# Performance work log

Measured on AMD Instinct MI355X. Metric: run time of the kernel, lower is better.

Reference implementation:

```python
import jax, jax.numpy as jnp
import numpy as np

EMBED_DIM = 1024
NUM_HEADS = 16
HEAD_DIM = EMBED_DIM // NUM_HEADS
SCALING = HEAD_DIM ** -0.5
TGT, BSZ = 1024, 4


def setup_inputs() -> dict:
    key = jax.random.key(0)
    ks = jax.random.split(key, 8)
    query = jax.random.normal(ks[0], (TGT, BSZ, EMBED_DIM), dtype=jnp.float32)
    key_padding_mask = jax.random.randint(ks[1], (BSZ, TGT), 0, 2, dtype=jnp.int32)
    attn_mask = jax.random.normal(ks[2], (TGT, TGT), dtype=jnp.float32)
    attn_bias = jax.random.normal(ks[3], (BSZ * NUM_HEADS, TGT, TGT), dtype=jnp.float32)
    W_in = jax.random.normal(ks[4], (3 * EMBED_DIM, EMBED_DIM), dtype=jnp.float32) * 0.02
    b_in = jnp.zeros((3 * EMBED_DIM,), dtype=jnp.float32)
    W_out = jax.random.normal(ks[5], (EMBED_DIM, EMBED_DIM), dtype=jnp.float32) * 0.02
    b_out = jnp.zeros((EMBED_DIM,), dtype=jnp.float32)
    return {"query": query, "key_padding_mask": key_padding_mask,
            "attn_mask": attn_mask, "attn_bias": attn_bias,
            "W_in": W_in, "b_in": b_in, "W_out": W_out, "b_out": b_out}


def reference(query, key_padding_mask, attn_mask, attn_bias, W_in, b_in, W_out, b_out):
    tgt_len, bsz, embed_dim = query.shape
    # in_proj: (T,B,C) @ W_in.T -> (T,B,3C), chunk into q,k,v
    qkv = jnp.einsum('tbc,ec->tbe', query, W_in) + b_in
    q, k, v = jnp.split(qkv, 3, axis=-1)
    # reshape to (B*H, T, D)
    def to_bh(x):
        return x.reshape(tgt_len, bsz * NUM_HEADS, HEAD_DIM).transpose(1, 0, 2)
    q = to_bh(q) * SCALING
    k = to_bh(k)
    v = to_bh(v)
    src_len = k.shape[1]
    # scores: (B*H, T, S)
    attn_weights = jnp.einsum('ntd,nsd->nts', q, k)
    attn_weights = attn_weights + attn_mask[None, :, :]
    kpm = key_padding_mask.astype(bool)  # (B, S), True = pad
    aw = attn_weights.reshape(bsz, NUM_HEADS, tgt_len, src_len)
    aw = jnp.where(kpm[:, None, None, :], -jnp.inf, aw)
    attn_weights = aw.reshape(bsz * NUM_HEADS, tgt_len, src_len)
    attn_weights = attn_weights + attn_bias
    attn_probs = jax.nn.softmax(attn_weights, axis=-1)
    attn = jnp.einsum('nts,nsd->ntd', attn_probs, v)
    attn = attn.transpose(1, 0, 2).reshape(tgt_len, bsz, embed_dim)
    out = jnp.einsum('tbc,ec->tbe', attn, W_out) + b_out
    return out
```

## Files before the change

### kernel.cpp

```cpp
#include <hip/hip_runtime.h>

#define T_LEN 1024
#define B_SZ 4
#define EMB 1024
#define NH 16
#define HD 64
#define QKV_LD 3072

typedef _Float16 f16;
typedef __attribute__((ext_vector_type(8))) _Float16 f16x8;
typedef __attribute__((ext_vector_type(4))) _Float16 f16x4;
typedef __attribute__((ext_vector_type(4))) float f32x4;

__device__ __forceinline__ void gload16(const f16* g, f16* l) {
    __builtin_amdgcn_global_load_lds(
        (const __attribute__((address_space(1))) void*)g,
        (__attribute__((address_space(3))) void*)l, 16, 0, 0);
}

#define N4_Q  (4096 * 1024 / 4)
#define N4_WI (3072 * 1024 / 4)
#define N4_WO (1024 * 1024 / 4)
__global__ __launch_bounds__(256) void cvt_all(
    const float* __restrict__ q, const float* __restrict__ wi,
    const float* __restrict__ wo, f16* __restrict__ q16,
    f16* __restrict__ wi16, f16* __restrict__ wo16)
{
    int i = blockIdx.x * 256 + threadIdx.x;
    const float* src; f16* dst; int off;
    if (i < N4_Q)             { src = q;  dst = q16;  off = i; }
    else if (i < N4_Q + N4_WI){ src = wi; dst = wi16; off = i - N4_Q; }
    else                      { src = wo; dst = wo16; off = i - N4_Q - N4_WI; }
    float4 v = ((const float4*)src)[off];
    f16x4 h = { (f16)v.x, (f16)v.y, (f16)v.z, (f16)v.w };
    ((f16x4*)dst)[off] = h;
}

template<bool OUT_HALF>
__global__ __launch_bounds__(256) void gemm_ct(
    const f16* __restrict__ Wt, const f16* __restrict__ Xa,
    const float* __restrict__ bias, void* __restrict__ Out,
    int K, int ldo)
{
    __shared__ f16 As[128 * 32];
    __shared__ f16 Bs[128 * 32];
    const int tid = threadIdx.x;
    const int wv = tid >> 6, lane = tid & 63;
    const int lq = lane & 15, quad = lane >> 4;
    const int m0 = blockIdx.x * 128, n0 = blockIdx.y * 128;
    const int wm = (wv >> 1) * 64, wn = (wv & 1) * 64;

    const int s1 = tid, s2 = 256 + tid;
    const f16* a1 = Wt + (size_t)(m0 + (s1 >> 2)) * K + (s1 & 3) * 8;
    const f16* a2 = Wt + (size_t)(m0 + (s2 >> 2)) * K + (s2 & 3) * 8;
    const f16* b1 = Xa + (size_t)(n0 + (s1 >> 2)) * K + (s1 & 3) * 8;
    const f16* b2 = Xa + (size_t)(n0 + (s2 >> 2)) * K + (s2 & 3) * 8;
    f16* lA1 = As + s1 * 8; f16* lA2 = As + s2 * 8;
    f16* lB1 = Bs + s1 * 8; f16* lB2 = Bs + s2 * 8;

    f32x4 acc[4][4];
#pragma unroll
    for (int i = 0; i < 4; ++i)
#pragma unroll
        for (int j = 0; j < 4; ++j) acc[i][j] = (f32x4){0.f, 0.f, 0.f, 0.f};

    for (int k0 = 0; k0 < K; k0 += 32) {
        __syncthreads();
        gload16(a1 + k0, lA1);
        gload16(a2 + k0, lA2);
        gload16(b1 + k0, lB1);
        gload16(b2 + k0, lB2);
        __syncthreads();
        f16x8 af[4], bf[4];
#pragma unroll
        for (int t = 0; t < 4; ++t) {
            af[t] = *(const f16x8*)&As[(wm + t * 16 + lq) * 32 + quad * 8];
            bf[t] = *(const f16x8*)&Bs[(wn + t * 16 + lq) * 32 + quad * 8];
        }
#pragma unroll
        for (int mt = 0; mt < 4; ++mt)
#pragma unroll
            for (int nt = 0; nt < 4; ++nt)
                acc[mt][nt] = __builtin_amdgcn_mfma_f32_16x16x32_f16(
                    af[mt], bf[nt], acc[mt][nt], 0, 0, 0);
    }

#pragma unroll
    for (int mt = 0; mt < 4; ++mt) {
        const int e0 = m0 + wm + mt * 16 + quad * 4;
        const float4 bb = *(const float4*)(bias + e0);
#pragma unroll
        for (int nt = 0; nt < 4; ++nt) {
            const int xr = n0 + wn + nt * 16 + lq;
            if (OUT_HALF) {
                f16x4 h = { (f16)(acc[mt][nt][0] + bb.x), (f16)(acc[mt][nt][1] + bb.y),
                            (f16)(acc[mt][nt][2] + bb.z), (f16)(acc[mt][nt][3] + bb.w) };
                *(f16x4*)((f16*)Out + (size_t)xr * ldo + e0) = h;
            } else {
                float4 o = { acc[mt][nt][0] + bb.x, acc[mt][nt][1] + bb.y,
                             acc[mt][nt][2] + bb.z, acc[mt][nt][3] + bb.w };
                *(float4*)((float*)Out + (size_t)xr * ldo + e0) = o;
            }
        }
    }
}

__global__ __launch_bounds__(256) void vtrans(
    const f16* __restrict__ qkv, f16* __restrict__ Vth)
{
    __shared__ f16 Ls[256 * 66];
    const int bh = blockIdx.x;
    const int t0 = blockIdx.y * 256;
    const int b = bh >> 4, hh = bh & 15;
    const int tid = threadIdx.x;

#pragma unroll
    for (int p = 0; p < 8; ++p) {
        const int g = p * 2048 + tid * 8;
        const int ti = g >> 6, dj = g & 63;
        f16x8 v = *(const f16x8*)(qkv + (size_t)((t0 + ti) * 4 + b) * QKV_LD + 2048 + hh * 64 + dj);
        *(f16x8*)&Ls[ti * 66 + dj] = v;
    }
    __syncthreads();
#pragma unroll
    for (int p = 0; p < 8; ++p) {
        const int g = p * 2048 + tid * 8;
        const int d = g >> 8, tt = g & 255;
        f16x8 o;
#pragma unroll
        for (int j = 0; j < 8; ++j) o[j] = Ls[(tt + j) * 66 + d];
        *(f16x8*)(Vth + (size_t)bh * 65536 + (size_t)d * 1024 + t0 + tt) = o;
    }
}

__global__ __launch_bounds__(256, 3) void attn_v5(
    const f16* __restrict__ qkv, const f16* __restrict__ Vth,
    const int* __restrict__ kpm, const float* __restrict__ attn_mask,
    const float* __restrict__ attn_bias, f16* __restrict__ ctx)
{
    const int LDP = 72;
    __shared__ f16 Ps[4 * 16 * LDP];

    const int tid = threadIdx.x;
    const int wv = tid >> 6, lane = tid & 63;
    const int lq = lane & 15, quad = lane >> 4;
    const int q0 = blockIdx.x * 64;
    const int bh = blockIdx.y;
    const int b = bh >> 4, hh = bh & 15;
    f16* Pw = Ps + wv * 16 * LDP;

    const int t = q0 + wv * 16 + lq;
    const float* mrow = attn_mask + (size_t)t * T_LEN;
    const float* brow = attn_bias + ((size_t)bh * T_LEN + t) * T_LEN;
    const int* kpr = kpm + b * T_LEN;
    const f16* Vb = Vth + (size_t)bh * 65536;

    f16x8 bq[2];
    {
        const f16* qrow = qkv + (size_t)(t * 4 + b) * QKV_LD + hh * 64;
        bq[0] = *(const f16x8*)(qrow + quad * 8);
        bq[1] = *(const f16x8*)(qrow + 32 + quad * 8);
    }

    float m_i = -1e30f, l_i = 0.0f;
    f32x4 O[4];
#pragma unroll
    for (int dt = 0; dt < 4; ++dt) O[dt] = (f32x4){0.f, 0.f, 0.f, 0.f};

    f32x4 bcur[4];
#pragma unroll
    for (int st = 0; st < 4; ++st)
        bcur[st] = __builtin_nontemporal_load((const f32x4*)(brow + st * 16 + quad * 4));

#pragma unroll 1
    for (int sh = 0; sh < T_LEN; sh += 64) {
        f32x4 bnxt[4];
        if (sh + 64 < T_LEN) {
#pragma unroll
            for (int st = 0; st < 4; ++st)
                bnxt[st] = __builtin_nontemporal_load(
                    (const f32x4*)(brow + sh + 64 + st * 16 + quad * 4));
        }

        f16x8 ak[2][4];
#pragma unroll
        for (int ks = 0; ks < 2; ++ks)
#pragma unroll
            for (int st = 0; st < 4; ++st)
                ak[ks][st] = *(const f16x8*)(qkv
                    + (size_t)((sh + st * 16 + lq) * 4 + b) * QKV_LD
                    + EMB + hh * 64 + ks * 32 + quad * 8);

        f32x4 m4[4]; int4 kp4[4];
#pragma unroll
        for (int st = 0; st < 4; ++st) {
            const int sb = sh + st * 16 + quad * 4;
            m4[st] = *(const f32x4*)(mrow + sb);
            kp4[st] = *(const int4*)(kpr + sb);
        }

        f32x4 sacc[4];
#pragma unroll
        for (int st = 0; st < 4; ++st) sacc[st] = (f32x4){0.f, 0.f, 0.f, 0.f};
        __builtin_amdgcn_s_setprio(1);
#pragma unroll
        for (int ks = 0; ks < 2; ++ks)
#pragma unroll
            for (int st = 0; st < 4; ++st)
                sacc[st] = __builtin_amdgcn_mfma_f32_16x16x32_f16(
                    ak[ks][st], bq[ks], sacc[st], 0, 0, 0);
        __builtin_amdgcn_s_setprio(0);

        f16x8 av[2][4];
#pragma unroll
        for (int ks = 0; ks < 2; ++ks)
#pragma unroll
            for (int dt = 0; dt < 4; ++dt)
                av[ks][dt] = *(const f16x8*)(Vb + (size_t)(dt * 16 + lq) * 1024
                                             + sh + ks * 32 + quad * 8);

        float sv[4][4];
        float rm = -1e30f;
#pragma unroll
        for (int st = 0; st < 4; ++st) {
            const int kv[4] = {kp4[st].x, kp4[st].y, kp4[st].z, kp4[st].w};
#pragma unroll
            for (int r = 0; r < 4; ++r) {
                const float x = sacc[st][r] * 0.125f + m4[st][r] + bcur[st][r];
                sv[st][r] = kv[r] ? -1e30f : x;
                rm = fmaxf(rm, sv[st][r]);
            }
        }
        rm = fmaxf(rm, __shfl_xor(rm, 16));
        rm = fmaxf(rm, __shfl_xor(rm, 32));

        const bool skip = __all(rm <= m_i + 8.0f);
        float alpha;
        if (skip) {
            alpha = 1.0f;
        } else {
            const float mn = fmaxf(m_i, rm);
            alpha = __expf(m_i - mn);
            m_i = mn;
        }

        __builtin_amdgcn_wave_barrier();
        float rs = 0.0f;
#pragma unroll
        for (int st = 0; st < 4; ++st) {
            f16x4 pv;
#pragma unroll
            for (int r = 0; r < 4; ++r) {
                const float p = __expf(sv[st][r] - m_i);
                rs += p;
                pv[r] = (f16)p;
            }
            *(f16x4*)&Pw[lq * LDP + st * 16 + quad * 4] = pv;
        }
        rs += __shfl_xor(rs, 16);
        rs += __shfl_xor(rs, 32);
        l_i = l_i * alpha + rs;

        if (!skip) {
            float aB[4];
#pragma unroll
            for (int r = 0; r < 4; ++r) aB[r] = __shfl(alpha, quad * 4 + r, 16);
#pragma unroll
            for (int dt = 0; dt < 4; ++dt)
#pragma unroll
                for (int r = 0; r < 4; ++r) O[dt][r] *= aB[r];
        }

        __builtin_amdgcn_wave_barrier();

        __builtin_amdgcn_s_setprio(1);
#pragma unroll
        for (int ks = 0; ks < 2; ++ks) {
            const f16x8 ap = *(const f16x8*)&Pw[lq * LDP + ks * 32 + quad * 8];
#pragma unroll
            for (int dt = 0; dt < 4; ++dt)
                O[dt] = __builtin_amdgcn_mfma_f32_16x16x32_f16(
                    ap, av[ks][dt], O[dt], 0, 0, 0);
        }
        __builtin_amdgcn_s_setprio(0);

#pragma unroll
        for (int st = 0; st < 4; ++st) bcur[st] = bnxt[st];
    }

    float lB[4];
#pragma unroll
    for (int r = 0; r < 4; ++r) lB[r] = __shfl(l_i, quad * 4 + r, 16);
#pragma unroll
    for (int r = 0; r < 4; ++r) {
        const float inv = 1.0f / lB[r];
        const int tt = q0 + wv * 16 + quad * 4 + r;
#pragma unroll
        for (int dt = 0; dt < 4; ++dt)
            ctx[((size_t)tt * B_SZ + b) * EMB + hh * HD + dt * 16 + lq] = (f16)(O[dt][r] * inv);
    }
}

extern "C" void kernel_launch(void* const* d_in, const int* in_sizes, int n_in,
                              void* d_out, int out_size, void* d_ws, size_t ws_size,
                              hipStream_t stream)
{
    const float* query     = (const float*)d_in[0];
    const int*   kpm       = (const int*)  d_in[1];
    const float* attn_mask = (const float*)d_in[2];
    const float* attn_bias = (const float*)d_in[3];
    const float* W_in      = (const float*)d_in[4];
    const float* b_in      = (const float*)d_in[5];
    const float* W_out     = (const float*)d_in[6];
    const float* b_out     = (const float*)d_in[7];
    float* out = (float*)d_out;

    f16* q16    = (f16*)d_ws;
    f16* win16  = q16    + (size_t)4096 * 1024;
    f16* wout16 = win16  + (size_t)3072 * 1024;
    f16* qkv16  = wout16 + (size_t)1024 * 1024;
    f16* Vth    = qkv16  + (size_t)4096 * 3072;
    f16* ctx16  = Vth    + (size_t)64 * 65536;

    cvt_all<<<(N4_Q + N4_WI + N4_WO) / 256, 256, 0, stream>>>(
        query, W_in, W_out, q16, win16, wout16);

    dim3 g1(3072 / 128, 4096 / 128);
    gemm_ct<true><<<g1, 256, 0, stream>>>(win16, q16, b_in, qkv16, 1024, QKV_LD);

    dim3 gv(64, 4);
    vtrans<<<gv, 256, 0, stream>>>(qkv16, Vth);

    dim3 g2(T_LEN / 64, B_SZ * NH);
    attn_v5<<<g2, 256, 0, stream>>>(qkv16, Vth, kpm, attn_mask, attn_bias, ctx16);

    dim3 g3(1024 / 128, 4096 / 128);
    gemm_ct<false><<<g3, 256, 0, stream>>>(wout16, ctx16, b_out, out, 1024, 1024);
}
```

Measured before the change: 579.2 us.

## Split attention key range across two wave groups and prefold padding into mask

The attention kernel now uses 512 threads per block. Two groups of four waves each process half of the key sequence, and their partial softmax states (max, sum, output) are merged through shared memory at the end. A new prepass kernel folds the key padding mask into a per-batch copy of the additive attention mask. This removes the int mask loads and selects from the inner loop. The split is meant to raise parallelism and hide the latency of the memory-bound bias stream, at the cost of an extra 16MB mask buffer, an extra kernel launch and the merge step.

```diff
diff --git a/kernel.cpp b/kernel.cpp
--- a/kernel.cpp
+++ b/kernel.cpp
@@ -34,6 +34,21 @@
     float4 v = ((const float4*)src)[off];
     f16x4 h = { (f16)v.x, (f16)v.y, (f16)v.z, (f16)v.w };
     ((f16x4*)dst)[off] = h;
+}
+
+__global__ __launch_bounds__(256) void maskfold(
+    const float* __restrict__ attn_mask, const int* __restrict__ kpm,
+    float* __restrict__ maskc)
+{
+    const int i = blockIdx.x * 256 + threadIdx.x;
+    const int s4 = i & 255;
+    const int t = (i >> 8) & 1023;
+    const int b = i >> 18;
+    float4 m = ((const float4*)(attn_mask + (size_t)t * T_LEN))[s4];
+    int4 k = ((const int4*)(kpm + b * T_LEN))[s4];
+    float4 o = { k.x ? -1e30f : m.x, k.y ? -1e30f : m.y,
+                 k.z ? -1e30f : m.z, k.w ? -1e30f : m.w };
+    ((float4*)(maskc + ((size_t)b * T_LEN + t) * T_LEN))[s4] = o;
 }
 
 template<bool OUT_HALF>
@@ -133,26 +148,30 @@
     }
 }
 
-__global__ __launch_bounds__(256, 3) void attn_v5(
+__global__ __launch_bounds__(512, 6) void attn_v6(
     const f16* __restrict__ qkv, const f16* __restrict__ Vth,
-    const int* __restrict__ kpm, const float* __restrict__ attn_mask,
-    const float* __restrict__ attn_bias, f16* __restrict__ ctx)
+    const float* __restrict__ maskc, const float* __restrict__ attn_bias,
+    f16* __restrict__ ctx)
 {
     const int LDP = 72;
-    __shared__ f16 Ps[4 * 16 * LDP];
+    __shared__ f16 Ps[8 * 16 * LDP];
+    __shared__ float Osh[4][16][66];
+    __shared__ float Msh[4][16];
+    __shared__ float Lsh[4][16];
 
     const int tid = threadIdx.x;
     const int wv = tid >> 6, lane = tid & 63;
+    const int wq = wv & 3, half = wv >> 2;
     const int lq = lane & 15, quad = lane >> 4;
     const int q0 = blockIdx.x * 64;
     const int bh = blockIdx.y;
     const int b = bh >> 4, hh = bh & 15;
     f16* Pw = Ps + wv * 16 * LDP;
 
-    const int t = q0 + wv * 16 + lq;
-    const float* mrow = attn_mask + (size_t)t * T_LEN;
+    const int t = q0 + wq * 16 + lq;
+    const int S0 = half * 512;
+    const float* mrow = maskc + ((size_t)b * T_LEN + t) * T_LEN;
     const float* brow = attn_bias + ((size_t)bh * T_LEN + t) * T_LEN;
-    const int* kpr = kpm + b * T_LEN;
     const f16* Vb = Vth + (size_t)bh * 65536;
 
     f16x8 bq[2];
@@ -170,12 +189,13 @@
     f32x4 bcur[4];
 #pragma unroll
     for (int st = 0; st < 4; ++st)
-        bcur[st] = __builtin_nontemporal_load((const f32x4*)(brow + st * 16 + quad * 4));
+        bcur[st] = __builtin_nontemporal_load(
+            (const f32x4*)(brow + S0 + st * 16 + quad * 4));
 
 #pragma unroll 1
-    for (int sh = 0; sh < T_LEN; sh += 64) {
+    for (int sh = S0; sh < S0 + 512; sh += 64) {
         f32x4 bnxt[4];
-        if (sh + 64 < T_LEN) {
+        if (sh + 64 < S0 + 512) {
 #pragma unroll
             for (int st = 0; st < 4; ++st)
                 bnxt[st] = __builtin_nontemporal_load(
@@ -191,13 +211,10 @@
                     + (size_t)((sh + st * 16 + lq) * 4 + b) * QKV_LD
                     + EMB + hh * 64 + ks * 32 + quad * 8);
 
-        f32x4 m4[4]; int4 kp4[4];
-#pragma unroll
-        for (int st = 0; st < 4; ++st) {
-            const int sb = sh + st * 16 + quad * 4;
-            m4[st] = *(const f32x4*)(mrow + sb);
-            kp4[st] = *(const int4*)(kpr + sb);
-        }
+        f32x4 m4[4];
+#pragma unroll
+        for (int st = 0; st < 4; ++st)
+            m4[st] = *(const f32x4*)(mrow + sh + st * 16 + quad * 4);
 
         f32x4 sacc[4];
 #pragma unroll
@@ -223,11 +240,9 @@
         float rm = -1e30f;
 #pragma unroll
         for (int st = 0; st < 4; ++st) {
-            const int kv[4] = {kp4[st].x, kp4[st].y, kp4[st].z, kp4[st].w};
 #pragma unroll
             for (int r = 0; r < 4; ++r) {
-                const float x = sacc[st][r] * 0.125f + m4[st][r] + bcur[st][r];
-                sv[st][r] = kv[r] ? -1e30f : x;
+                sv[st][r] = sacc[st][r] * 0.125f + m4[st][r] + bcur[st][r];
                 rm = fmaxf(rm, sv[st][r]);
             }
         }
@@ -288,16 +303,38 @@
         for (int st = 0; st < 4; ++st) bcur[st] = bnxt[st];
     }
 
-    float lB[4];
-#pragma unroll
-    for (int r = 0; r < 4; ++r) lB[r] = __shfl(l_i, quad * 4 + r, 16);
-#pragma unroll
-    for (int r = 0; r < 4; ++r) {
-        const float inv = 1.0f / lB[r];
-        const int tt = q0 + wv * 16 + quad * 4 + r;
+    if (half == 1) {
 #pragma unroll
         for (int dt = 0; dt < 4; ++dt)
-            ctx[((size_t)tt * B_SZ + b) * EMB + hh * HD + dt * 16 + lq] = (f16)(O[dt][r] * inv);
+#pragma unroll
+            for (int r = 0; r < 4; ++r)
+                Osh[wq][quad * 4 + r][dt * 16 + lq] = O[dt][r];
+        if (lane < 16) { Msh[wq][lq] = m_i; Lsh[wq][lq] = l_i; }
+    }
+    __syncthreads();
+    if (half == 0) {
+        const float mB = Msh[wq][lq], lB2 = Lsh[wq][lq];
+        const float mm = fmaxf(m_i, mB);
+        const float eA = __expf(m_i - mm), eB = __expf(mB - mm);
+        const float lT = l_i * eA + lB2 * eB;
+        float eAr[4], eBr[4], lTr[4];
+#pragma unroll
+        for (int r = 0; r < 4; ++r) {
+            eAr[r] = __shfl(eA, quad * 4 + r, 16);
+            eBr[r] = __shfl(eB, quad * 4 + r, 16);
+            lTr[r] = __shfl(lT, quad * 4 + r, 16);
+        }
+#pragma unroll
+        for (int r = 0; r < 4; ++r) {
+            const float inv = 1.0f / lTr[r];
+            const int tt = q0 + wq * 16 + quad * 4 + r;
+#pragma unroll
+            for (int dt = 0; dt < 4; ++dt) {
+                const float o = (O[dt][r] * eAr[r]
+                               + Osh[wq][quad * 4 + r][dt * 16 + lq] * eBr[r]) * inv;
+                ctx[((size_t)tt * B_SZ + b) * EMB + hh * HD + dt * 16 + lq] = (f16)o;
+            }
+        }
     }
 }
 
@@ -321,10 +358,13 @@
     f16* qkv16  = wout16 + (size_t)1024 * 1024;
     f16* Vth    = qkv16  + (size_t)4096 * 3072;
     f16* ctx16  = Vth    + (size_t)64 * 65536;
+    float* maskc = (float*)(ctx16 + (size_t)4096 * 1024);
 
     cvt_all<<<(N4_Q + N4_WI + N4_WO) / 256, 256, 0, stream>>>(
         query, W_in, W_out, q16, win16, wout16);
 
+    maskfold<<<(4 * 1024 * 256) / 256, 256, 0, stream>>>(attn_mask, kpm, maskc);
+
     dim3 g1(3072 / 128, 4096 / 128);
     gemm_ct<true><<<g1, 256, 0, stream>>>(win16, q16, b_in, qkv16, 1024, QKV_LD);
 
@@ -332,7 +372,7 @@
     vtrans<<<gv, 256, 0, stream>>>(qkv16, Vth);
 
     dim3 g2(T_LEN / 64, B_SZ * NH);
-    attn_v5<<<g2, 256, 0, stream>>>(qkv16, Vth, kpm, attn_mask, attn_bias, ctx16);
+    attn_v6<<<g2, 512, 0, stream>>>(qkv16, Vth, maskc, attn_bias, ctx16);
 
     dim3 g3(1024 / 128, 4096 / 128);
     gemm_ct<false><<<g3, 256, 0, stream>>>(wout16, ctx16, b_out, out, 1024, 1024);
```

New measurement: 836.4 us. +44.4%, slower.
